# Kernel tuning notes

Measured on AMD Instinct MI355X. Metric: run time of the kernel, lower is better.

Reference implementation:

```python
import jax, jax.numpy as jnp
import numpy as np
import math

P = 7          # patch / kernel size (must be odd for onion-peeling: N = 1+4*m*(m+1) = P*P)
EPS = 1e-6
EPS_W = 0.5

def _ball_dirs():
    u = [np.array([[1.0, 0.0]])]
    s = [np.zeros(1)]
    for k in range(1, P // 2 + 1):
        n = 8 * k
        th = np.linspace(0.0, 2.0 * math.pi * (1.0 - 1.0 / n), n)
        u.append(np.stack([np.cos(th), np.sin(th)], 1))
        s.append(np.full(n, k / (P // 2)))
    return (np.concatenate(u, 0).astype(np.float32), np.concatenate(s).astype(np.float32))

_U, _S = _ball_dirs()  # [N,2], [N], N == P*P == 49

def _forward(x, metric_w, metric_b, proj_w, proj_b):
    B, C, H, W = x.shape
    Hp, Wp = H // P, W // P
    u = jnp.asarray(_U)
    s = jnp.asarray(_S)
    # metric net: strided conv -> 7 params per patch
    params = jax.lax.conv_general_dilated(
        x, metric_w, (P, P), 'VALID',
        dimension_numbers=('NCHW', 'OIHW', 'NCHW')) + metric_b[None, :, None, None]
    v_raw = jnp.moveaxis(params[:, :2], 1, -1)                      # [B,Hp,Wp,2]
    v = v_raw / jnp.maximum(jnp.linalg.norm(v_raw, axis=-1, keepdims=True), 1e-12)
    eig = 2.0 * jax.nn.sigmoid(jnp.moveaxis(params[:, 2:4], 1, -1))  # [B,Hp,Wp,2]
    scale = 0.5 + 1.5 * jax.nn.sigmoid(jnp.moveaxis(params[:, 4:5], 1, -1))
    eig = eig * scale
    vp = jnp.stack([-v[..., 1], v[..., 0]], -1)
    R = jnp.stack([v, vp], -1)                                      # [B,Hp,Wp,2,2] (columns v, v_perp)
    M = R @ (eig[..., None] * jnp.swapaxes(R, -1, -2))              # R diag(eig) R^T
    w = params[:, 5:7]                                              # [B,2,Hp,Wp]
    w = w * (1.0 - EPS_W) * jax.nn.sigmoid(jnp.linalg.norm(w, axis=1, keepdims=True))
    # Finsler-Randers norm F(u) = sqrt(u^T M u + eps) + w.u for all N unit dirs
    quad = jnp.einsum('nj,bhwij,ni->bnhw', u, M, u)                 # [B,N,Hp,Wp]
    drift = jnp.einsum('bihw,ni->bnhw', w, u)
    F_u = jnp.sqrt(quad + EPS) + drift
    y = (u[None, :, :, None, None] / (F_u[:, :, None] + EPS)
         * s[None, :, None, None, None])                            # [B,N,2,Hp,Wp]
    y = y.reshape(B, P, P, 2, Hp, Wp)[:, :, :, ::-1]                # flip last coord pair (x,y)->(y,x)
    gi = jnp.arange(P, dtype=x.dtype) - P // 2
    grid = jnp.stack(jnp.meshgrid(gi, gi, indexing='ij'), -1)       # [P,P,2]
    off = y - grid[None, :, :, :, None, None]                       # [B,P,P,2,Hp,Wp]
    off_y = jnp.transpose(off[:, :, :, 0], (0, 3, 4, 1, 2))         # [B,Hp,Wp,P,P]
    off_x = jnp.transpose(off[:, :, :, 1], (0, 3, 4, 1, 2))
    base_h = (jnp.arange(Hp, dtype=x.dtype) * P)[None, :, None, None, None]
    base_w = (jnp.arange(Wp, dtype=x.dtype) * P)[None, None, :, None, None]
    ki = jnp.arange(P, dtype=x.dtype)
    py = off_y + base_h + ki[None, None, None, :, None]             # sample rows
    px = off_x + base_w + ki[None, None, None, None, :]             # sample cols
    # bilinear sampling with zero padding (torchvision deform_conv2d semantics)
    y0 = jnp.floor(py)
    x0 = jnp.floor(px)
    wy = py - y0
    wx = px - x0

    def gather(yi, xi):
        valid = (yi >= 0) & (yi <= H - 1) & (xi >= 0) & (xi <= W - 1)
        yc = jnp.clip(yi, 0, H - 1).astype(jnp.int32)
        xc = jnp.clip(xi, 0, W - 1).astype(jnp.int32)
        vals = jax.vmap(lambda img, yy, xx: img[:, yy, xx])(x, yc, xc)  # [B,C,Hp,Wp,P,P]
        return vals * valid[:, None].astype(x.dtype)

    sampled = (gather(y0, x0) * ((1 - wy) * (1 - wx))[:, None]
               + gather(y0, x0 + 1) * ((1 - wy) * wx)[:, None]
               + gather(y0 + 1, x0) * (wy * (1 - wx))[:, None]
               + gather(y0 + 1, x0 + 1) * (wy * wx)[:, None])       # [B,C,Hp,Wp,P,P]
    out = jnp.einsum('bchwij,ecij->behw', sampled, proj_w) + proj_b[None, :, None, None]
    return jnp.moveaxis(out.reshape(B, out.shape[1], -1), 1, 2)     # [B, Hp*Wp, E]

def setup_inputs():
    key = jax.random.key(0)
    k0, k1, k2 = jax.random.split(key, 3)
    B, C, H, W, E = 64, 3, 224, 224, 384
    x = jax.random.normal(k0, (B, C, H, W), jnp.float32)
    metric_w = jax.random.normal(k1, (7, C, P, P), jnp.float32) / math.sqrt(C * P * P)
    metric_b = jnp.zeros((7,), jnp.float32)
    proj_w = jax.random.normal(k2, (E, C, P, P), jnp.float32) / (P * math.sqrt(C))
    proj_b = jnp.zeros((E,), jnp.float32)
    return {"x": x, "metric_w": metric_w, "metric_b": metric_b,
            "proj_w": proj_w, "proj_b": proj_b}

def reference(x, metric_w, metric_b, proj_w, proj_b):
    return _forward(x, metric_w, metric_b, proj_w, proj_b)
```

## Files before the change

### kernel.cpp

```cpp
#include <hip/hip_runtime.h>
#include <math.h>

#define PP   7
#define NDIR 49
#define CIN  3
#define KK   147
#define KPAD 160
#define EE   384
#define HH   224
#define WW   224
#define GG   16
#define TB   256
#define SSTR 17
#define NPX  112

typedef __attribute__((ext_vector_type(8))) __bf16 bf16x8;
typedef __attribute__((ext_vector_type(4))) float  f32x4;

__device__ __forceinline__ float sigmoidf_(float v) {
    return 1.0f / (1.0f + expf(-v));
}

__global__ void pack_kernel(const float* __restrict__ x,
                            const float* __restrict__ pw,
                            float* __restrict__ xp,
                            unsigned short* __restrict__ pwB,
                            int npix4) {
    int idx = blockIdx.x * blockDim.x + threadIdx.x;
    if (idx < EE * KPAD) {
        int e = idx / KPAD;
        int k = idx - e * KPAD;
        float v = (k < KK) ? pw[e * KK + k] : 0.0f;
        __bf16 h = (__bf16)v;
        pwB[idx] = *(unsigned short*)&h;
    }
    if (idx < npix4) {
        const int ppi = HH * WW / 4;
        int b = idx / ppi;
        int p = (idx - b * ppi) * 4;
        const float* xb = x + (size_t)b * (CIN * HH * WW) + p;
        f32x4 r0 = *(const f32x4*)(xb);
        f32x4 r1 = *(const f32x4*)(xb + HH * WW);
        f32x4 r2 = *(const f32x4*)(xb + 2 * HH * WW);
        float* op = xp + ((size_t)b * (HH * WW) + p) * 4;
        #pragma unroll
        for (int i = 0; i < 4; ++i) {
            f32x4 v = {r0[i], r1[i], r2[i], 0.0f};
            *(f32x4*)(op + i * 4) = v;
        }
    }
}

__device__ __forceinline__ void geom_(int item, int row0, int col0,
                                      const float dirs[NDIR][3], const float der[GG][5],
                                      int& g, int& n,
                                      int& o00, int& o01, int& o10, int& o11,
                                      float& c00, float& c01, float& c10, float& c11) {
    g = item / NDIR;
    n = item - g * NDIR;
    float u0 = dirs[n][0], u1 = dirs[n][1], s = dirs[n][2];
    float M00 = der[g][0], M01 = der[g][1], M11 = der[g][2];
    float w0 = der[g][3], w1 = der[g][4];
    float quad  = u0 * u0 * M00 + 2.0f * u0 * u1 * M01 + u1 * u1 * M11;
    float drift = w0 * u0 + w1 * u1;
    float F = sqrtf(quad + 1e-6f) + drift;
    float r = s / (F + 1e-6f);
    float py = (float)(row0 + 3) + u1 * r;
    float px = (float)(col0 + g * PP + 3) + u0 * r;
    float y0f = floorf(py), x0f = floorf(px);
    float y1f = y0f + 1.0f, x1f = x0f + 1.0f;
    float wy = py - y0f, wx = px - x0f;
    c00 = (1.0f - wy) * (1.0f - wx);
    c01 = (1.0f - wy) * wx;
    c10 = wy * (1.0f - wx);
    c11 = wy * wx;
    bool vy0 = (y0f >= 0.0f) && (y0f <= (float)(HH - 1));
    bool vy1 = (y1f >= 0.0f) && (y1f <= (float)(HH - 1));
    bool vx0 = (x0f >= 0.0f) && (x0f <= (float)(WW - 1));
    bool vx1 = (x1f >= 0.0f) && (x1f <= (float)(WW - 1));
    c00 *= (vy0 && vx0) ? 1.0f : 0.0f;
    c01 *= (vy0 && vx1) ? 1.0f : 0.0f;
    c10 *= (vy1 && vx0) ? 1.0f : 0.0f;
    c11 *= (vy1 && vx1) ? 1.0f : 0.0f;
    int iy0 = (int)fminf(fmaxf(y0f, 0.0f), (float)(HH - 1));
    int iy1 = (int)fminf(fmaxf(y1f, 0.0f), (float)(HH - 1));
    int ix0 = (int)fminf(fmaxf(x0f, 0.0f), (float)(WW - 1));
    int ix1 = (int)fminf(fmaxf(x1f, 0.0f), (float)(WW - 1));
    o00 = iy0 * WW + ix0; o01 = iy0 * WW + ix1;
    o10 = iy1 * WW + ix0; o11 = iy1 * WW + ix1;
}

__launch_bounds__(TB, 6)
__global__ void fused_kernel(const float* __restrict__ x,
                             const float* __restrict__ xp,
                             const float* __restrict__ mw,
                             const float* __restrict__ mb,
                             const unsigned short* __restrict__ pwB,
                             const float* __restrict__ pb,
                             float* __restrict__ out) {
    __shared__ float mws[7 * KK];
    __shared__ float dirs[NDIR][3];
    __shared__ float par_s[GG][8];
    __shared__ float der_s[GG][5];
    __shared__ __align__(16) float buf[3136];

    const int t   = threadIdx.x;
    const int blk = blockIdx.x;
    const int b   = blk >> 6;
    const int rem = blk & 63;
    const int hp  = rem >> 1;
    const int wp0 = (rem & 1) * GG;
    const size_t m0 = (size_t)blk * GG;
    const int row0 = hp * PP;
    const int col0 = wp0 * PP;

    for (int i = t; i < 7 * KK; i += TB) mws[i] = mw[i];
    if (t >= 64 && t < 64 + NDIR) {
        int n = t - 64;
        float u0, u1, s;
        if (n == 0)      { u0 = 1.0f; u1 = 0.0f; s = 0.0f; }
        else if (n < 9)  { float th = (float)(n - 1)  * 0.78539816339744831f; u0 = cosf(th); u1 = sinf(th); s = 0.33333334f; }
        else if (n < 25) { float th = (float)(n - 9)  * 0.39269908169872414f; u0 = cosf(th); u1 = sinf(th); s = 0.66666669f; }
        else             { float th = (float)(n - 25) * 0.26179938779914941f; u0 = cosf(th); u1 = sinf(th); s = 1.0f; }
        dirs[n][0] = u0; dirs[n][1] = u1; dirs[n][2] = s;
    }

    const size_t pbase = (size_t)b * (HH * WW);
    for (int item = t; item < 7 * NPX; item += TB) {
        int i = item / NPX, px = item - i * NPX;
        f32x4 v = *(const f32x4*)(xp + (pbase + (size_t)(row0 + i) * WW + col0 + px) * 4);
        *(f32x4*)&buf[item * 4] = v;
    }
    __syncthreads();

    if (t < 112) {
        int prm = t >> 4, g = t & 15;
        const float* wrow = &mws[prm * KK];
        float acc0 = 0.0f, acc1 = 0.0f, acc2 = 0.0f;
        #pragma unroll 1
        for (int i = 0; i < 7; ++i) {
            const float* bp = &buf[(i * NPX + g * 7) * 4];
            const float* w0 = &wrow[i * 7];
            const float* w1 = &wrow[49 + i * 7];
            const float* w2 = &wrow[98 + i * 7];
            #pragma unroll
            for (int j = 0; j < 7; ++j) {
                acc0 = fmaf(bp[j * 4 + 0], w0[j], acc0);
                acc1 = fmaf(bp[j * 4 + 1], w1[j], acc1);
                acc2 = fmaf(bp[j * 4 + 2], w2[j], acc2);
            }
        }
        par_s[g][prm] = mb[prm] + acc0 + acc1 + acc2;
    }
    __syncthreads();

    if (t < GG) {
        float a0 = par_s[t][0], a1 = par_s[t][1], a2 = par_s[t][2], a3 = par_s[t][3];
        float a4 = par_s[t][4], a5 = par_s[t][5], a6 = par_s[t][6];
        float nrm = sqrtf(a0 * a0 + a1 * a1);
        float inv = 1.0f / fmaxf(nrm, 1e-12f);
        float v0 = a0 * inv, v1 = a1 * inv;
        float e0 = 2.0f * sigmoidf_(a2);
        float e1 = 2.0f * sigmoidf_(a3);
        float sc = 0.5f + 1.5f * sigmoidf_(a4);
        e0 *= sc; e1 *= sc;
        float wn  = sqrtf(a5 * a5 + a6 * a6);
        float wsc = 0.5f * sigmoidf_(wn);
        der_s[t][0] = e0 * v0 * v0 + e1 * v1 * v1;
        der_s[t][1] = (e0 - e1) * v0 * v1;
        der_s[t][2] = e0 * v1 * v1 + e1 * v0 * v0;
        der_s[t][3] = a5 * wsc;
        der_s[t][4] = a6 * wsc;
    }
    __syncthreads();

    #pragma unroll
    for (int half = 0; half < 2; ++half) {
        int itemA = half * 512 + t;
        int itemB = itemA + 256;
        bool validB = (itemB < GG * NDIR);
        int itemBc = validB ? itemB : 0;

        int gA, nA, a00, a01, a10, a11;  float cA00, cA01, cA10, cA11;
        int gB, nB, b00, b01, b10, b11;  float cB00, cB01, cB10, cB11;
        geom_(itemA,  row0, col0, dirs, der_s, gA, nA, a00, a01, a10, a11, cA00, cA01, cA10, cA11);
        geom_(itemBc, row0, col0, dirs, der_s, gB, nB, b00, b01, b10, b11, cB00, cB01, cB10, cB11);

        f32x4 qa0 = *(const f32x4*)(xp + (pbase + (size_t)a00) * 4);
        f32x4 qa1 = *(const f32x4*)(xp + (pbase + (size_t)a01) * 4);
        f32x4 qa2 = *(const f32x4*)(xp + (pbase + (size_t)a10) * 4);
        f32x4 qa3 = *(const f32x4*)(xp + (pbase + (size_t)a11) * 4);
        f32x4 qb0 = *(const f32x4*)(xp + (pbase + (size_t)b00) * 4);
        f32x4 qb1 = *(const f32x4*)(xp + (pbase + (size_t)b01) * 4);
        f32x4 qb2 = *(const f32x4*)(xp + (pbase + (size_t)b10) * 4);
        f32x4 qb3 = *(const f32x4*)(xp + (pbase + (size_t)b11) * 4);

        #pragma unroll
        for (int c = 0; c < CIN; ++c) {
            buf[(c * NDIR + nA) * SSTR + gA] =
                qa0[c] * cA00 + qa1[c] * cA01 + qa2[c] * cA10 + qa3[c] * cA11;
        }
        if (validB) {
            #pragma unroll
            for (int c = 0; c < CIN; ++c) {
                buf[(c * NDIR + nB) * SSTR + gB] =
                    qb0[c] * cB00 + qb1[c] * cB01 + qb2[c] * cB10 + qb3[c] * cB11;
            }
        }
    }
    __syncthreads();

    const int lane = t & 63;
    const int wv   = t >> 6;
    const int nrow = lane & 15;
    const int hi   = lane >> 4;

    bf16x8 sfr[5];
    #pragma unroll
    for (int ks = 0; ks < 5; ++ks) {
        #pragma unroll
        for (int j = 0; j < 8; ++j) {
            int k = ks * 32 + hi * 8 + j;
            float v = (k < KK) ? buf[k * SSTR + nrow] : 0.0f;
            sfr[ks][j] = (__bf16)v;
        }
    }

    float* orow = out + (m0 + nrow) * EE;
    #pragma unroll
    for (int q = 0; q < 6; ++q) {
        int tile = wv * 6 + q;
        int erow = tile * 16 + nrow;
        const unsigned short* arow = pwB + (size_t)erow * KPAD + hi * 8;
        f32x4 acc = {0.0f, 0.0f, 0.0f, 0.0f};
        #pragma unroll
        for (int ks = 0; ks < 5; ++ks) {
            bf16x8 afr = *(const bf16x8*)&arow[ks * 32];
            acc = __builtin_amdgcn_mfma_f32_16x16x32_bf16(afr, sfr[ks], acc, 0, 0, 0);
        }
        int e0 = tile * 16 + hi * 4;
        f32x4 b4 = *(const f32x4*)&pb[e0];
        f32x4 o = acc + b4;
        *(f32x4*)&orow[e0] = o;
    }
}

__launch_bounds__(TB, 6)
__global__ void fused_planar_kernel(const float* __restrict__ x,
                                    const float* __restrict__ mw,
                                    const float* __restrict__ mb,
                                    const unsigned short* __restrict__ pwB,
                                    const float* __restrict__ pb,
                                    float* __restrict__ out) {
    __shared__ float mws[7 * KK];
    __shared__ float dirs[NDIR][3];
    __shared__ float par_s[GG][8];
    __shared__ float der_s[GG][5];
    __shared__ __align__(16) float buf[2512];

    const int t   = threadIdx.x;
    const int blk = blockIdx.x;
    const int b   = blk >> 6;
    const int rem = blk & 63;
    const int hp  = rem >> 1;
    const int wp0 = (rem & 1) * GG;
    const size_t m0 = (size_t)blk * GG;
    const int row0 = hp * PP;
    const int col0 = wp0 * PP;
    const float* xb = x + (size_t)b * (CIN * HH * WW);

    for (int i = t; i < 7 * KK; i += TB) mws[i] = mw[i];
    if (t >= 64 && t < 64 + NDIR) {
        int n = t - 64;
        float u0, u1, s;
        if (n == 0)      { u0 = 1.0f; u1 = 0.0f; s = 0.0f; }
        else if (n < 9)  { float th = (float)(n - 1)  * 0.78539816339744831f; u0 = cosf(th); u1 = sinf(th); s = 0.33333334f; }
        else if (n < 25) { float th = (float)(n - 9)  * 0.39269908169872414f; u0 = cosf(th); u1 = sinf(th); s = 0.66666669f; }
        else             { float th = (float)(n - 25) * 0.26179938779914941f; u0 = cosf(th); u1 = sinf(th); s = 1.0f; }
        dirs[n][0] = u0; dirs[n][1] = u1; dirs[n][2] = s;
    }
    for (int item = t; item < CIN * 7 * NPX; item += TB) {
        int c = item / (7 * NPX), r2 = item - c * (7 * NPX);
        int i = r2 / NPX, px = r2 - i * NPX;
        buf[item] = xb[(size_t)c * (HH * WW) + (size_t)(row0 + i) * WW + col0 + px];
    }
    __syncthreads();
    if (t < 112) {
        int prm = t >> 4, g = t & 15;
        const float* wrow = &mws[prm * KK];
        float acc0 = 0.0f, acc1 = 0.0f, acc2 = 0.0f;
        #pragma unroll 1
        for (int i = 0; i < 7; ++i) {
            const float* b0 = &buf[(0 * 7 + i) * NPX + g * 7];
            const float* b1 = &buf[(1 * 7 + i) * NPX + g * 7];
            const float* b2 = &buf[(2 * 7 + i) * NPX + g * 7];
            #pragma unroll
            for (int j = 0; j < 7; ++j) {
                acc0 = fmaf(b0[j], wrow[i * 7 + j], acc0);
                acc1 = fmaf(b1[j], wrow[49 + i * 7 + j], acc1);
                acc2 = fmaf(b2[j], wrow[98 + i * 7 + j], acc2);
            }
        }
        par_s[g][prm] = mb[prm] + acc0 + acc1 + acc2;
    }
    __syncthreads();
    if (t < GG) {
        float a0 = par_s[t][0], a1 = par_s[t][1], a2 = par_s[t][2], a3 = par_s[t][3];
        float a4 = par_s[t][4], a5 = par_s[t][5], a6 = par_s[t][6];
        float nrm = sqrtf(a0 * a0 + a1 * a1);
        float inv = 1.0f / fmaxf(nrm, 1e-12f);
        float v0 = a0 * inv, v1 = a1 * inv;
        float e0 = 2.0f * sigmoidf_(a2);
        float e1 = 2.0f * sigmoidf_(a3);
        float sc = 0.5f + 1.5f * sigmoidf_(a4);
        e0 *= sc; e1 *= sc;
        float wn  = sqrtf(a5 * a5 + a6 * a6);
        float wsc = 0.5f * sigmoidf_(wn);
        der_s[t][0] = e0 * v0 * v0 + e1 * v1 * v1;
        der_s[t][1] = (e0 - e1) * v0 * v1;
        der_s[t][2] = e0 * v1 * v1 + e1 * v0 * v0;
        der_s[t][3] = a5 * wsc;
        der_s[t][4] = a6 * wsc;
    }
    __syncthreads();
    for (int item = t; item < GG * NDIR; item += TB) {
        int g, n, o00, o01, o10, o11; float c00, c01, c10, c11;
        geom_(item, row0, col0, dirs, der_s, g, n, o00, o01, o10, o11, c00, c01, c10, c11);
        #pragma unroll
        for (int c = 0; c < CIN; ++c) {
            const float* xc = xb + c * (HH * WW);
            buf[(c * NDIR + n) * SSTR + g] =
                xc[o00] * c00 + xc[o01] * c01 + xc[o10] * c10 + xc[o11] * c11;
        }
    }
    __syncthreads();
    const int lane = t & 63;
    const int wv   = t >> 6;
    const int nrow = lane & 15;
    const int hi   = lane >> 4;
    bf16x8 sfr[5];
    #pragma unroll
    for (int ks = 0; ks < 5; ++ks) {
        #pragma unroll
        for (int j = 0; j < 8; ++j) {
            int k = ks * 32 + hi * 8 + j;
            float v = (k < KK) ? buf[k * SSTR + nrow] : 0.0f;
            sfr[ks][j] = (__bf16)v;
        }
    }
    float* orow = out + (m0 + nrow) * EE;
    #pragma unroll
    for (int q = 0; q < 6; ++q) {
        int tile = wv * 6 + q;
        int erow = tile * 16 + nrow;
        const unsigned short* arow = pwB + (size_t)erow * KPAD + hi * 8;
        f32x4 acc = {0.0f, 0.0f, 0.0f, 0.0f};
        #pragma unroll
        for (int ks = 0; ks < 5; ++ks) {
            bf16x8 afr = *(const bf16x8*)&arow[ks * 32];
            acc = __builtin_amdgcn_mfma_f32_16x16x32_bf16(afr, sfr[ks], acc, 0, 0, 0);
        }
        int e0 = tile * 16 + hi * 4;
        f32x4 b4 = *(const f32x4*)&pb[e0];
        f32x4 o = acc + b4;
        *(f32x4*)&orow[e0] = o;
    }
}

extern "C" void kernel_launch(void* const* d_in, const int* in_sizes, int n_in,
                              void* d_out, int out_size, void* d_ws, size_t ws_size,
                              hipStream_t stream) {
    const float* x  = (const float*)d_in[0];
    const float* mw = (const float*)d_in[1];
    const float* mb = (const float*)d_in[2];
    const float* pw = (const float*)d_in[3];
    const float* pb = (const float*)d_in[4];
    float* out = (float*)d_out;

    unsigned short* pwB = (unsigned short*)d_ws;
    float* xp = (float*)((char*)d_ws + (size_t)(1 << 17));

    const int B = in_sizes[0] / (CIN * HH * WW);
    const int npix = B * HH * WW;
    const int npix4 = npix / 4;
    const size_t need = (size_t)(1 << 17) + (size_t)npix * 4 * sizeof(float);
    const bool packed = ws_size >= need;

    if (packed) {
        int grid = (npix4 > EE * KPAD ? npix4 : EE * KPAD);
        pack_kernel<<<(grid + 255) / 256, 256, 0, stream>>>(x, pw, xp, pwB, npix4);
        fused_kernel<<<B * 64, TB, 0, stream>>>(x, xp, mw, mb, pwB, pb, out);
    } else {
        pack_kernel<<<(EE * KPAD + 255) / 256, 256, 0, stream>>>(x, pw, xp, pwB, 0);
        fused_planar_kernel<<<B * 64, TB, 0, stream>>>(x, mw, mb, pwB, pb, out);
    }
}
```

Before: 206.1 us.

## Repack metric weights and sampled buffer for vectorized LDS access, raise occupancy

Adds a packed, channel-interleaved copy of the metric conv weights built in the pack kernel, so the per-patch conv can read weights and pixels as float4 from LDS. The sampled-patch buffer moves to a row-per-patch layout with zero padding, letting the MFMA operand load use two float4 reads instead of eight strided scalar reads. The two-items-per-thread unrolled gather becomes a simple strided loop, and launch bounds go from 6 to 8 waves. This trades some memory-level parallelism in the gather for lower register pressure and fewer LDS instructions, and the new padded layout may introduce LDS bank conflicts.

```diff
diff --git a/kernel.cpp b/kernel.cpp
--- a/kernel.cpp
+++ b/kernel.cpp
@@ -11,8 +11,10 @@
 #define WW   224
 #define GG   16
 #define TB   256
+#define NPX  112
+#define WSTR 208
+#define SROW 164
 #define SSTR 17
-#define NPX  112
 
 typedef __attribute__((ext_vector_type(8))) __bf16 bf16x8;
 typedef __attribute__((ext_vector_type(4))) float  f32x4;
@@ -23,8 +25,10 @@
 
 __global__ void pack_kernel(const float* __restrict__ x,
                             const float* __restrict__ pw,
+                            const float* __restrict__ mw,
                             float* __restrict__ xp,
                             unsigned short* __restrict__ pwB,
+                            float* __restrict__ mwg,
                             int npix4) {
     int idx = blockIdx.x * blockDim.x + threadIdx.x;
     if (idx < EE * KPAD) {
@@ -33,6 +37,15 @@
         float v = (k < KK) ? pw[e * KK + k] : 0.0f;
         __bf16 h = (__bf16)v;
         pwB[idx] = *(unsigned short*)&h;
+    }
+    if (idx < 7 * WSTR) {
+        int prm = idx / WSTR, r = idx - prm * WSTR;
+        float v = 0.0f;
+        if (r < 196) {
+            int q = r >> 2, c = r & 3;
+            if (c < 3) v = mw[prm * KK + c * 49 + q];
+        }
+        mwg[idx] = v;
     }
     if (idx < npix4) {
         const int ppi = HH * WW / 4;
@@ -51,54 +64,14 @@
     }
 }
 
-__device__ __forceinline__ void geom_(int item, int row0, int col0,
-                                      const float dirs[NDIR][3], const float der[GG][5],
-                                      int& g, int& n,
-                                      int& o00, int& o01, int& o10, int& o11,
-                                      float& c00, float& c01, float& c10, float& c11) {
-    g = item / NDIR;
-    n = item - g * NDIR;
-    float u0 = dirs[n][0], u1 = dirs[n][1], s = dirs[n][2];
-    float M00 = der[g][0], M01 = der[g][1], M11 = der[g][2];
-    float w0 = der[g][3], w1 = der[g][4];
-    float quad  = u0 * u0 * M00 + 2.0f * u0 * u1 * M01 + u1 * u1 * M11;
-    float drift = w0 * u0 + w1 * u1;
-    float F = sqrtf(quad + 1e-6f) + drift;
-    float r = s / (F + 1e-6f);
-    float py = (float)(row0 + 3) + u1 * r;
-    float px = (float)(col0 + g * PP + 3) + u0 * r;
-    float y0f = floorf(py), x0f = floorf(px);
-    float y1f = y0f + 1.0f, x1f = x0f + 1.0f;
-    float wy = py - y0f, wx = px - x0f;
-    c00 = (1.0f - wy) * (1.0f - wx);
-    c01 = (1.0f - wy) * wx;
-    c10 = wy * (1.0f - wx);
-    c11 = wy * wx;
-    bool vy0 = (y0f >= 0.0f) && (y0f <= (float)(HH - 1));
-    bool vy1 = (y1f >= 0.0f) && (y1f <= (float)(HH - 1));
-    bool vx0 = (x0f >= 0.0f) && (x0f <= (float)(WW - 1));
-    bool vx1 = (x1f >= 0.0f) && (x1f <= (float)(WW - 1));
-    c00 *= (vy0 && vx0) ? 1.0f : 0.0f;
-    c01 *= (vy0 && vx1) ? 1.0f : 0.0f;
-    c10 *= (vy1 && vx0) ? 1.0f : 0.0f;
-    c11 *= (vy1 && vx1) ? 1.0f : 0.0f;
-    int iy0 = (int)fminf(fmaxf(y0f, 0.0f), (float)(HH - 1));
-    int iy1 = (int)fminf(fmaxf(y1f, 0.0f), (float)(HH - 1));
-    int ix0 = (int)fminf(fmaxf(x0f, 0.0f), (float)(WW - 1));
-    int ix1 = (int)fminf(fmaxf(x1f, 0.0f), (float)(WW - 1));
-    o00 = iy0 * WW + ix0; o01 = iy0 * WW + ix1;
-    o10 = iy1 * WW + ix0; o11 = iy1 * WW + ix1;
-}
-
-__launch_bounds__(TB, 6)
-__global__ void fused_kernel(const float* __restrict__ x,
-                             const float* __restrict__ xp,
-                             const float* __restrict__ mw,
+__launch_bounds__(TB, 8)
+__global__ void fused_kernel(const float* __restrict__ xp,
+                             const float* __restrict__ mwg,
                              const float* __restrict__ mb,
                              const unsigned short* __restrict__ pwB,
                              const float* __restrict__ pb,
                              float* __restrict__ out) {
-    __shared__ float mws[7 * KK];
+    __shared__ __align__(16) float mwp_s[7 * WSTR];
     __shared__ float dirs[NDIR][3];
     __shared__ float par_s[GG][8];
     __shared__ float der_s[GG][5];
@@ -114,7 +87,8 @@
     const int row0 = hp * PP;
     const int col0 = wp0 * PP;
 
-    for (int i = t; i < 7 * KK; i += TB) mws[i] = mw[i];
+    for (int i4 = t; i4 < 7 * WSTR / 4; i4 += TB)
+        *(f32x4*)&mwp_s[i4 * 4] = *(const f32x4*)&mwg[i4 * 4];
     if (t >= 64 && t < 64 + NDIR) {
         int n = t - 64;
         float u0, u1, s;
@@ -135,19 +109,19 @@
 
     if (t < 112) {
         int prm = t >> 4, g = t & 15;
-        const float* wrow = &mws[prm * KK];
+        const float* wrow = &mwp_s[prm * WSTR];
         float acc0 = 0.0f, acc1 = 0.0f, acc2 = 0.0f;
         #pragma unroll 1
         for (int i = 0; i < 7; ++i) {
             const float* bp = &buf[(i * NPX + g * 7) * 4];
-            const float* w0 = &wrow[i * 7];
-            const float* w1 = &wrow[49 + i * 7];
-            const float* w2 = &wrow[98 + i * 7];
+            const float* wp = &wrow[i * 28];
             #pragma unroll
             for (int j = 0; j < 7; ++j) {
-                acc0 = fmaf(bp[j * 4 + 0], w0[j], acc0);
-                acc1 = fmaf(bp[j * 4 + 1], w1[j], acc1);
-                acc2 = fmaf(bp[j * 4 + 2], w2[j], acc2);
+                f32x4 pix = *(const f32x4*)&bp[j * 4];
+                f32x4 w4  = *(const f32x4*)&wp[j * 4];
+                acc0 = fmaf(pix[0], w4[0], acc0);
+                acc1 = fmaf(pix[1], w4[1], acc1);
+                acc2 = fmaf(pix[2], w4[2], acc2);
             }
         }
         par_s[g][prm] = mb[prm] + acc0 + acc1 + acc2;
@@ -172,40 +146,51 @@
         der_s[t][3] = a5 * wsc;
         der_s[t][4] = a6 * wsc;
     }
-    __syncthreads();
-
-    #pragma unroll
-    for (int half = 0; half < 2; ++half) {
-        int itemA = half * 512 + t;
-        int itemB = itemA + 256;
-        bool validB = (itemB < GG * NDIR);
-        int itemBc = validB ? itemB : 0;
-
-        int gA, nA, a00, a01, a10, a11;  float cA00, cA01, cA10, cA11;
-        int gB, nB, b00, b01, b10, b11;  float cB00, cB01, cB10, cB11;
-        geom_(itemA,  row0, col0, dirs, der_s, gA, nA, a00, a01, a10, a11, cA00, cA01, cA10, cA11);
-        geom_(itemBc, row0, col0, dirs, der_s, gB, nB, b00, b01, b10, b11, cB00, cB01, cB10, cB11);
-
-        f32x4 qa0 = *(const f32x4*)(xp + (pbase + (size_t)a00) * 4);
-        f32x4 qa1 = *(const f32x4*)(xp + (pbase + (size_t)a01) * 4);
-        f32x4 qa2 = *(const f32x4*)(xp + (pbase + (size_t)a10) * 4);
-        f32x4 qa3 = *(const f32x4*)(xp + (pbase + (size_t)a11) * 4);
-        f32x4 qb0 = *(const f32x4*)(xp + (pbase + (size_t)b00) * 4);
-        f32x4 qb1 = *(const f32x4*)(xp + (pbase + (size_t)b01) * 4);
-        f32x4 qb2 = *(const f32x4*)(xp + (pbase + (size_t)b10) * 4);
-        f32x4 qb3 = *(const f32x4*)(xp + (pbase + (size_t)b11) * 4);
-
+    for (int z = t; z < GG * (SROW - KK); z += TB) {
+        int g = z / (SROW - KK), r = z - g * (SROW - KK);
+        buf[g * SROW + KK + r] = 0.0f;
+    }
+    __syncthreads();
+
+    for (int item = t; item < GG * NDIR; item += TB) {
+        int g = item / NDIR;
+        int n = item - g * NDIR;
+        float u0 = dirs[n][0], u1 = dirs[n][1], s = dirs[n][2];
+        float M00 = der_s[g][0], M01 = der_s[g][1], M11 = der_s[g][2];
+        float w0 = der_s[g][3], w1 = der_s[g][4];
+        float quad  = u0 * u0 * M00 + 2.0f * u0 * u1 * M01 + u1 * u1 * M11;
+        float drift = w0 * u0 + w1 * u1;
+        float F = sqrtf(quad + 1e-6f) + drift;
+        float r = s / (F + 1e-6f);
+        float py = (float)(row0 + 3) + u1 * r;
+        float px = (float)(col0 + g * PP + 3) + u0 * r;
+        float y0f = floorf(py), x0f = floorf(px);
+        float y1f = y0f + 1.0f, x1f = x0f + 1.0f;
+        float wy = py - y0f, wx = px - x0f;
+        float c00 = (1.0f - wy) * (1.0f - wx);
+        float c01 = (1.0f - wy) * wx;
+        float c10 = wy * (1.0f - wx);
+        float c11 = wy * wx;
+        bool vy0 = (y0f >= 0.0f) && (y0f <= (float)(HH - 1));
+        bool vy1 = (y1f >= 0.0f) && (y1f <= (float)(HH - 1));
+        bool vx0 = (x0f >= 0.0f) && (x0f <= (float)(WW - 1));
+        bool vx1 = (x1f >= 0.0f) && (x1f <= (float)(WW - 1));
+        c00 *= (vy0 && vx0) ? 1.0f : 0.0f;
+        c01 *= (vy0 && vx1) ? 1.0f : 0.0f;
+        c10 *= (vy1 && vx0) ? 1.0f : 0.0f;
+        c11 *= (vy1 && vx1) ? 1.0f : 0.0f;
+        int iy0 = (int)fminf(fmaxf(y0f, 0.0f), (float)(HH - 1));
+        int iy1 = (int)fminf(fmaxf(y1f, 0.0f), (float)(HH - 1));
+        int ix0 = (int)fminf(fmaxf(x0f, 0.0f), (float)(WW - 1));
+        int ix1 = (int)fminf(fmaxf(x1f, 0.0f), (float)(WW - 1));
+        f32x4 q00 = *(const f32x4*)(xp + (pbase + (size_t)(iy0 * WW + ix0)) * 4);
+        f32x4 q01 = *(const f32x4*)(xp + (pbase + (size_t)(iy0 * WW + ix1)) * 4);
+        f32x4 q10 = *(const f32x4*)(xp + (pbase + (size_t)(iy1 * WW + ix0)) * 4);
+        f32x4 q11 = *(const f32x4*)(xp + (pbase + (size_t)(iy1 * WW + ix1)) * 4);
         #pragma unroll
         for (int c = 0; c < CIN; ++c) {
-            buf[(c * NDIR + nA) * SSTR + gA] =
-                qa0[c] * cA00 + qa1[c] * cA01 + qa2[c] * cA10 + qa3[c] * cA11;
-        }
-        if (validB) {
-            #pragma unroll
-            for (int c = 0; c < CIN; ++c) {
-                buf[(c * NDIR + nB) * SSTR + gB] =
-                    qb0[c] * cB00 + qb1[c] * cB01 + qb2[c] * cB10 + qb3[c] * cB11;
-            }
+            buf[g * SROW + c * NDIR + n] =
+                q00[c] * c00 + q01[c] * c01 + q10[c] * c10 + q11[c] * c11;
         }
     }
     __syncthreads();
@@ -216,14 +201,15 @@
     const int hi   = lane >> 4;
 
     bf16x8 sfr[5];
+    const float* srow = &buf[nrow * SROW];
     #pragma unroll
     for (int ks = 0; ks < 5; ++ks) {
-        #pragma unroll
-        for (int j = 0; j < 8; ++j) {
-            int k = ks * 32 + hi * 8 + j;
-            float v = (k < KK) ? buf[k * SSTR + nrow] : 0.0f;
-            sfr[ks][j] = (__bf16)v;
-        }
+        f32x4 lo = *(const f32x4*)&srow[ks * 32 + hi * 8];
+        f32x4 hv = *(const f32x4*)&srow[ks * 32 + hi * 8 + 4];
+        #pragma unroll
+        for (int j = 0; j < 4; ++j) sfr[ks][j] = (__bf16)lo[j];
+        #pragma unroll
+        for (int j = 0; j < 4; ++j) sfr[ks][4 + j] = (__bf16)hv[j];
     }
 
     float* orow = out + (m0 + nrow) * EE;
@@ -324,8 +310,38 @@
     }
     __syncthreads();
     for (int item = t; item < GG * NDIR; item += TB) {
-        int g, n, o00, o01, o10, o11; float c00, c01, c10, c11;
-        geom_(item, row0, col0, dirs, der_s, g, n, o00, o01, o10, o11, c00, c01, c10, c11);
+        int g = item / NDIR;
+        int n = item - g * NDIR;
+        float u0 = dirs[n][0], u1 = dirs[n][1], s = dirs[n][2];
+        float M00 = der_s[g][0], M01 = der_s[g][1], M11 = der_s[g][2];
+        float w0 = der_s[g][3], w1 = der_s[g][4];
+        float quad  = u0 * u0 * M00 + 2.0f * u0 * u1 * M01 + u1 * u1 * M11;
+        float drift = w0 * u0 + w1 * u1;
+        float F = sqrtf(quad + 1e-6f) + drift;
+        float r = s / (F + 1e-6f);
+        float py = (float)(row0 + 3) + u1 * r;
+        float px = (float)(col0 + g * PP + 3) + u0 * r;
+        float y0f = floorf(py), x0f = floorf(px);
+        float y1f = y0f + 1.0f, x1f = x0f + 1.0f;
+        float wy = py - y0f, wx = px - x0f;
+        float c00 = (1.0f - wy) * (1.0f - wx);
+        float c01 = (1.0f - wy) * wx;
+        float c10 = wy * (1.0f - wx);
+        float c11 = wy * wx;
+        bool vy0 = (y0f >= 0.0f) && (y0f <= (float)(HH - 1));
+        bool vy1 = (y1f >= 0.0f) && (y1f <= (float)(HH - 1));
+        bool vx0 = (x0f >= 0.0f) && (x0f <= (float)(WW - 1));
+        bool vx1 = (x1f >= 0.0f) && (x1f <= (float)(WW - 1));
+        c00 *= (vy0 && vx0) ? 1.0f : 0.0f;
+        c01 *= (vy0 && vx1) ? 1.0f : 0.0f;
+        c10 *= (vy1 && vx0) ? 1.0f : 0.0f;
+        c11 *= (vy1 && vx1) ? 1.0f : 0.0f;
+        int iy0 = (int)fminf(fmaxf(y0f, 0.0f), (float)(HH - 1));
+        int iy1 = (int)fminf(fmaxf(y1f, 0.0f), (float)(HH - 1));
+        int ix0 = (int)fminf(fmaxf(x0f, 0.0f), (float)(WW - 1));
+        int ix1 = (int)fminf(fmaxf(x1f, 0.0f), (float)(WW - 1));
+        int o00 = iy0 * WW + ix0, o01 = iy0 * WW + ix1;
+        int o10 = iy1 * WW + ix0, o11 = iy1 * WW + ix1;
         #pragma unroll
         for (int c = 0; c < CIN; ++c) {
             const float* xc = xb + c * (HH * WW);
@@ -378,7 +394,8 @@
     float* out = (float*)d_out;
 
     unsigned short* pwB = (unsigned short*)d_ws;
-    float* xp = (float*)((char*)d_ws + (size_t)(1 << 17));
+    float* mwg = (float*)((char*)d_ws + (size_t)(EE * KPAD) * 2);
+    float* xp  = (float*)((char*)d_ws + (size_t)(1 << 17));
 
     const int B = in_sizes[0] / (CIN * HH * WW);
     const int npix = B * HH * WW;
@@ -388,10 +405,10 @@
 
     if (packed) {
         int grid = (npix4 > EE * KPAD ? npix4 : EE * KPAD);
-        pack_kernel<<<(grid + 255) / 256, 256, 0, stream>>>(x, pw, xp, pwB, npix4);
-        fused_kernel<<<B * 64, TB, 0, stream>>>(x, xp, mw, mb, pwB, pb, out);
+        pack_kernel<<<(grid + 255) / 256, 256, 0, stream>>>(x, pw, mw, xp, pwB, mwg, npix4);
+        fused_kernel<<<B * 64, TB, 0, stream>>>(xp, mwg, mb, pwB, pb, out);
     } else {
-        pack_kernel<<<(EE * KPAD + 255) / 256, 256, 0, stream>>>(x, pw, xp, pwB, 0);
+        pack_kernel<<<(EE * KPAD + 255) / 256, 256, 0, stream>>>(x, pw, mw, xp, pwB, mwg, 0);
         fused_planar_kernel<<<B * 64, TB, 0, stream>>>(x, mw, mb, pwB, pb, out);
     }
 }
```

Result: no change. 204.2 us (-0.9%).
